# Kernel tuning notes

Measured on AMD Instinct MI355X. Metric: run time of the kernel, lower is better.

The kernel has to match this reference:

```python
import jax, jax.numpy as jnp
import numpy as np

B, C, H, W = 4, 3, 32, 32
N_IMAGES = 32
TIMESTEPS = 20


def _extract_patches(x, pad_mode):
    """3x3 patches at every spatial location. x: [B,C,H,W] -> [B,C,9,H,W]."""
    if pad_mode == 'wrap':
        xp = jnp.pad(x, ((0, 0), (0, 0), (1, 1), (1, 1)), mode='wrap')
    else:
        xp = jnp.pad(x, ((0, 0), (0, 0), (1, 1), (1, 1)))
    h, w = x.shape[2], x.shape[3]
    sl = [xp[:, :, di:di + h, dj:dj + w] for di in range(3) for dj in range(3)]
    return jnp.stack(sl, axis=2)  # [B,C,9,H,W], k = di*3+dj (torch unfold order)


def setup_inputs() -> dict:
    key = jax.random.key(0)
    k1, k2 = jax.random.split(key)
    x = jax.random.normal(k1, (B, C, H, W), dtype=jnp.float32)
    images = jax.random.uniform(k2, (N_IMAGES, C, H, W), dtype=jnp.float32)
    # linear beta schedule, as in _noise_buffers
    betas = jnp.linspace(1e-4, 0.02, TIMESTEPS, dtype=jnp.float32)
    alpha_cumprod = jnp.cumprod(1.0 - betas)
    mu_sched = jnp.sqrt(alpha_cumprod)
    sigma_sched = jnp.sqrt(1.0 - alpha_cumprod)
    return {"x": x, "images": images, "mu_sched": mu_sched,
            "sigma_sched": sigma_sched, "t": 10}


def reference(x, images, mu_sched, sigma_sched, t):
    mu = mu_sched[t]
    sigma = sigma_sched[t]
    b, c, h, w = x.shape

    # x-side: circular-padded 3x3 patches and their squared norms
    xp = _extract_patches(x, 'wrap').reshape(b, c * 9, h, w)   # [B,C*9,H,W]
    x_norms = jnp.sum(xp * xp, axis=1)                          # [B,H,W]

    # dataset-side: zero-padded 3x3 patches at every pixel of every image
    ip = _extract_patches(images, 'zeros')                      # [N,C,9,H,W]
    patches = ip.transpose(0, 3, 4, 1, 2).reshape(-1, c * 9)    # [P, C*9], P=N*H*W
    pnorms = jnp.sum(patches * patches, axis=1)                 # [P]
    pcenters = patches.reshape(-1, c, 9)[:, :, 4]               # [P,C] center pixel (1,1)

    # conv2d(x_pad, patches) == contraction over the C*9 patch axis
    conv = jnp.einsum('bkhw,pk->bphw', xp, patches)             # [B,P,H,W]

    inv2s2 = 1.0 / (2.0 * sigma * sigma)
    log_w = -(x_norms[:, None] - 2.0 * mu * conv
              + (mu * mu) * pnorms[None, :, None, None]) * inv2s2  # [B,P,H,W]

    # stable softmax-style weights over the patch axis (== online LSE result)
    m = jnp.max(log_w, axis=1)                                  # [B,H,W]
    wgt = jnp.exp(log_w - m[:, None])                           # [B,P,H,W]
    sum_w = jnp.sum(wgt, axis=1)                                # [B,H,W]

    # sum_p w * (x - mu * pcenter) = x*sum_w - mu * (w @ pcenters)
    wc = jnp.einsum('bphw,pc->bchw', wgt, pcenters)             # [B,C,H,W]
    sum_wd = x * sum_w[:, None] - mu * wc
    return -sum_wd / (sigma * sigma * sum_w[:, None])
```

## Files before the change

kernel.cpp:

```cpp
#include <hip/hip_runtime.h>
#include <cstddef>

#define P_TOTAL 32768
#define Q_TOTAL 4096
#define NSPLIT 128
#define KPS 256
#define TILES 16
#define QPERWG 256
#define NQG (Q_TOTAL / QPERWG)
#define GRID (NSPLIT * NQG)

typedef _Float16 half8 __attribute__((ext_vector_type(8)));
typedef float floatx4 __attribute__((ext_vector_type(4)));
typedef float floatx2 __attribute__((ext_vector_type(2)));

__device__ __forceinline__ float fexp2(float x) {
#if defined(__has_builtin) && __has_builtin(__builtin_amdgcn_exp2f)
    return __builtin_amdgcn_exp2f(x);
#else
    return exp2f(x);
#endif
}

__global__ __launch_bounds__(256) void qbuild_k(
    const float* __restrict__ x, _Float16* __restrict__ q16)
{
    int q = blockIdx.x * 256 + threadIdx.x;
    int b = q >> 10, rem = q & 1023, h = rem >> 5, w = rem & 31;
    const float* xb = x + (size_t)b * 3072;
    _Float16 row[32];
    #pragma unroll
    for (int c = 0; c < 3; c++)
      #pragma unroll
      for (int di = 0; di < 3; di++)
        #pragma unroll
        for (int dj = 0; dj < 3; dj++)
            row[c * 9 + di * 3 + dj] =
                (_Float16)xb[c * 1024 + ((h + di + 31) & 31) * 32 + ((w + dj + 31) & 31)];
    row[27] = (_Float16)1.0f;
    row[28] = (_Float16)0.f; row[29] = (_Float16)0.f;
    row[30] = (_Float16)0.f; row[31] = (_Float16)0.f;
    _Float16* qp = q16 + (size_t)q * 32;
    #pragma unroll
    for (int u = 0; u < 4; u++) ((float4*)qp)[u] = ((float4*)row)[u];
}

__global__ __launch_bounds__(256) void score_k(
    const _Float16* __restrict__ q16, const float* __restrict__ images,
    const float* __restrict__ mu_sched, const float* __restrict__ sigma_sched,
    const int* __restrict__ tptr, float* __restrict__ partials)
{
    __shared__ char lds[KPS * 64 + 3 * KPS * 4];
    float* ctrp = (float*)(lds + KPS * 64);
    int tid = threadIdx.x;
    int split = blockIdx.x >> 4;
    int qg    = blockIdx.x & 15;

    int t = tptr[0];
    float mu = mu_sched[t], sg = sigma_sched[t];
    const float LOG2E = 1.4426950408889634f;
    float inv2s2 = 1.0f / (2.0f * sg * sg);
    float s1     = 2.0f * mu * inv2s2 * LOG2E;
    float bscale = -mu * mu * inv2s2 * LOG2E;

    {
        int r = tid;
        int p = split * KPS + r;
        int n = p >> 10, rem = p & 1023, i = rem >> 5, j = rem & 31;
        const float* img = images + (size_t)n * 3072;
        _Float16 hrow[32];
        float pnorm = 0.f, c0 = 0.f, c1 = 0.f, c2 = 0.f;
        #pragma unroll
        for (int c = 0; c < 3; c++)
          #pragma unroll
          for (int di = 0; di < 3; di++)
            #pragma unroll
            for (int dj = 0; dj < 3; dj++) {
                int ii = i + di - 1, jj = j + dj - 1;
                float val = 0.f;
                if (ii >= 0 && ii < 32 && jj >= 0 && jj < 32)
                    val = img[c * 1024 + ii * 32 + jj];
                hrow[c * 9 + di * 3 + dj] = (_Float16)(val * s1);
                pnorm = fmaf(val, val, pnorm);
                if (di == 1 && dj == 1) { if (c == 0) c0 = val; else if (c == 1) c1 = val; else c2 = val; }
            }
        hrow[27] = (_Float16)(pnorm * bscale);
        hrow[28] = (_Float16)0.f; hrow[29] = (_Float16)0.f;
        hrow[30] = (_Float16)0.f; hrow[31] = (_Float16)0.f;
        int sw = (r >> 1) & 3;
        float4* src4 = (float4*)hrow;
        #pragma unroll
        for (int c = 0; c < 4; c++)
            *(float4*)(lds + r * 64 + ((c ^ sw) << 4)) = src4[c];
        ctrp[0 * KPS + r] = c0;
        ctrp[1 * KPS + r] = c1;
        ctrp[2 * KPS + r] = c2;
    }

    int lane = tid & 63, wid = tid >> 6;
    int col  = lane & 15, quad = lane >> 4;
    int qbase = qg * QPERWG + wid * 64;

    half8 qf[4];
    #pragma unroll
    for (int f = 0; f < 4; f++)
        qf[f] = *(const half8*)(q16 + (size_t)(qbase + f * 16 + col) * 32 + quad * 8);
    __syncthreads();

    int swc = (col >> 1) & 3;
    const char* abase = lds + col * 64 + ((quad ^ swc) << 4);

    floatx2 mx2[4];
    #pragma unroll
    for (int f = 0; f < 4; f++) mx2[f] = (floatx2){-3e38f, -3e38f};
    {
        #pragma unroll 4
        for (int tile = 0; tile < TILES; tile++) {
            half8 ak = *(const half8*)(abase + tile * 1024);
            #pragma unroll
            for (int f = 0; f < 4; f++) {
                floatx4 a = __builtin_amdgcn_mfma_f32_16x16x32_f16(
                    ak, qf[f], (floatx4){0.f, 0.f, 0.f, 0.f}, 0, 0, 0);
                floatx2 alo = __builtin_shufflevector(a, a, 0, 1);
                floatx2 ahi = __builtin_shufflevector(a, a, 2, 3);
                mx2[f] = __builtin_elementwise_max(
                    mx2[f], __builtin_elementwise_max(alo, ahi));
            }
        }
    }
    float mx[4];
    #pragma unroll
    for (int f = 0; f < 4; f++) {
        mx[f] = fmaxf(mx2[f].x, mx2[f].y);
        mx[f] = fmaxf(mx[f], __shfl_xor(mx[f], 16, 64));
        mx[f] = fmaxf(mx[f], __shfl_xor(mx[f], 32, 64));
    }
    floatx4 nmv[4];
    #pragma unroll
    for (int f = 0; f < 4; f++)
        nmv[f] = (floatx4){-mx[f], -mx[f], -mx[f], -mx[f]};

    floatx2 sv2[4], w02[4], w12[4], w22[4];
    #pragma unroll
    for (int f = 0; f < 4; f++) {
        sv2[f] = (floatx2){0.f, 0.f};
        w02[f] = sv2[f]; w12[f] = sv2[f]; w22[f] = sv2[f];
    }
    {
        #pragma unroll 2
        for (int tile = 0; tile < TILES; tile++) {
            half8 ak = *(const half8*)(abase + tile * 1024);
            int gr = tile * 16 + quad * 4;
            floatx4 c0q = *(const floatx4*)(ctrp + 0 * KPS + gr);
            floatx4 c1q = *(const floatx4*)(ctrp + 1 * KPS + gr);
            floatx4 c2q = *(const floatx4*)(ctrp + 2 * KPS + gr);
            floatx2 c0a = __builtin_shufflevector(c0q, c0q, 0, 1);
            floatx2 c0b = __builtin_shufflevector(c0q, c0q, 2, 3);
            floatx2 c1a = __builtin_shufflevector(c1q, c1q, 0, 1);
            floatx2 c1b = __builtin_shufflevector(c1q, c1q, 2, 3);
            floatx2 c2a = __builtin_shufflevector(c2q, c2q, 0, 1);
            floatx2 c2b = __builtin_shufflevector(c2q, c2q, 2, 3);
            #pragma unroll
            for (int f = 0; f < 4; f++) {
                floatx4 a = __builtin_amdgcn_mfma_f32_16x16x32_f16(ak, qf[f], nmv[f], 0, 0, 0);
                floatx2 e01 = {fexp2(a[0]), fexp2(a[1])};
                floatx2 e23 = {fexp2(a[2]), fexp2(a[3])};
                sv2[f] += e01 + e23;
                w02[f] = __builtin_elementwise_fma(e01, c0a, w02[f]);
                w02[f] = __builtin_elementwise_fma(e23, c0b, w02[f]);
                w12[f] = __builtin_elementwise_fma(e01, c1a, w12[f]);
                w12[f] = __builtin_elementwise_fma(e23, c1b, w12[f]);
                w22[f] = __builtin_elementwise_fma(e01, c2a, w22[f]);
                w22[f] = __builtin_elementwise_fma(e23, c2b, w22[f]);
            }
        }
    }

    #pragma unroll
    for (int f = 0; f < 4; f++) {
        float sv = sv2[f].x + sv2[f].y;
        float w0 = w02[f].x + w02[f].y;
        float w1 = w12[f].x + w12[f].y;
        float w2 = w22[f].x + w22[f].y;
        sv += __shfl_xor(sv, 16, 64);  sv += __shfl_xor(sv, 32, 64);
        w0 += __shfl_xor(w0, 16, 64);  w0 += __shfl_xor(w0, 32, 64);
        w1 += __shfl_xor(w1, 16, 64);  w1 += __shfl_xor(w1, 32, 64);
        w2 += __shfl_xor(w2, 16, 64);  w2 += __shfl_xor(w2, 32, 64);
        if (quad == 0) {
            size_t idx = (size_t)split * Q_TOTAL + qbase + f * 16 + col;
            partials[idx]                          = mx[f];
            partials[idx + (size_t)NSPLIT * Q_TOTAL]     = sv;
            partials[idx + (size_t)NSPLIT * Q_TOTAL * 2] = w0;
            partials[idx + (size_t)NSPLIT * Q_TOTAL * 3] = w1;
            partials[idx + (size_t)NSPLIT * Q_TOTAL * 4] = w2;
        }
    }
}

__global__ __launch_bounds__(256) void combine_k(
    const float* __restrict__ x, const float* __restrict__ partials,
    const float* __restrict__ mu_sched, const float* __restrict__ sigma_sched,
    const int* __restrict__ tptr, float* __restrict__ out)
{
    int q = blockIdx.x * 256 + threadIdx.x;
    int t = tptr[0];
    float mu = mu_sched[t], sg = sigma_sched[t];
    float inv_s2 = 1.0f / (sg * sg);

    const size_t PL = (size_t)NSPLIT * Q_TOTAL;
    float M = -3e38f, S = 0.f, W0 = 0.f, W1 = 0.f, W2 = 0.f;
    for (int sp = 0; sp < NSPLIT; sp++) {
        size_t idx = (size_t)sp * Q_TOTAL + q;
        float mval = partials[idx];
        float sval = partials[idx + PL];
        float w0v  = partials[idx + PL * 2];
        float w1v  = partials[idx + PL * 3];
        float w2v  = partials[idx + PL * 4];
        float mnew = fmaxf(M, mval);
        float sco = fexp2(M - mnew);
        float scn = fexp2(mval - mnew);
        S  = fmaf(S,  sco, sval * scn);
        W0 = fmaf(W0, sco, w0v * scn);
        W1 = fmaf(W1, sco, w1v * scn);
        W2 = fmaf(W2, sco, w2v * scn);
        M = mnew;
    }
    float invS = 1.0f / S;
    int b = q >> 10, rem = q & 1023;
    #pragma unroll
    for (int c = 0; c < 3; c++) {
        float Wc = (c == 0) ? W0 : (c == 1 ? W1 : W2);
        float xc = x[(size_t)b * 3072 + c * 1024 + rem];
        out[(size_t)b * 3072 + c * 1024 + rem] = -(xc - mu * Wc * invS) * inv_s2;
    }
}

extern "C" void kernel_launch(void* const* d_in, const int* in_sizes, int n_in,
                              void* d_out, int out_size, void* d_ws, size_t ws_size,
                              hipStream_t stream) {
    const float* x      = (const float*)d_in[0];
    const float* images = (const float*)d_in[1];
    const float* mu_s   = (const float*)d_in[2];
    const float* sg_s   = (const float*)d_in[3];
    const int*   tptr   = (const int*)d_in[4];
    float* out = (float*)d_out;

    float*    partials = (float*)d_ws;
    _Float16* q16      = (_Float16*)((char*)d_ws + (size_t)5 * NSPLIT * Q_TOTAL * 4);

    qbuild_k<<<Q_TOTAL / 256, 256, 0, stream>>>(x, q16);
    score_k<<<GRID, 256, 0, stream>>>(q16, images, mu_s, sg_s, tptr, partials);
    combine_k<<<Q_TOTAL / 256, 256, 0, stream>>>(
        x, partials, mu_s, sg_s, tptr, out);
}
```

Before: 120.7 us.

## Compute weighted sums with a second MFMA over fp16 exp weights via LDS

Replaces the per-lane FMA accumulation of sum_w and the weighted patch centers with a second MFMA. The exp weights are converted to fp16, staged in per-wave LDS, and multiplied against an LDS value matrix holding [1, c0, c1, c2] plus zero padding. This moves the reduction work from VALU onto matrix cores. In exchange it adds LDS round trips, lowers precision by storing the weights in fp16 with round-toward-zero, and increases LDS footprint, which may reduce occupancy.

```diff
diff --git a/kernel.cpp b/kernel.cpp
--- a/kernel.cpp
+++ b/kernel.cpp
@@ -6,13 +6,24 @@
 #define NSPLIT 128
 #define KPS 256
 #define TILES 16
+#define NGROUP 8
 #define QPERWG 256
 #define NQG (Q_TOTAL / QPERWG)
 #define GRID (NSPLIT * NQG)
 
+#define KEYS_B 16384
+#define VT_OFF KEYS_B
+#define VT_PITCH 528
+#define VT_ZERO (VT_OFF + 4 * VT_PITCH)
+#define P_OFF (VT_OFF + 2624)
+#define P_FRAG 1280
+#define P_WAVE (4 * P_FRAG)
+#define LDS_TOTAL (P_OFF + 4 * P_WAVE)
+
 typedef _Float16 half8 __attribute__((ext_vector_type(8)));
+typedef __fp16 fp16x2 __attribute__((ext_vector_type(2)));
+typedef __fp16 fp16x4 __attribute__((ext_vector_type(4)));
 typedef float floatx4 __attribute__((ext_vector_type(4)));
-typedef float floatx2 __attribute__((ext_vector_type(2)));
 
 __device__ __forceinline__ float fexp2(float x) {
 #if defined(__has_builtin) && __has_builtin(__builtin_amdgcn_exp2f)
@@ -50,8 +61,7 @@
     const float* __restrict__ mu_sched, const float* __restrict__ sigma_sched,
     const int* __restrict__ tptr, float* __restrict__ partials)
 {
-    __shared__ char lds[KPS * 64 + 3 * KPS * 4];
-    float* ctrp = (float*)(lds + KPS * 64);
+    __shared__ char lds[LDS_TOTAL];
     int tid = threadIdx.x;
     int split = blockIdx.x >> 4;
     int qg    = blockIdx.x & 15;
@@ -92,9 +102,12 @@
         #pragma unroll
         for (int c = 0; c < 4; c++)
             *(float4*)(lds + r * 64 + ((c ^ sw) << 4)) = src4[c];
-        ctrp[0 * KPS + r] = c0;
-        ctrp[1 * KPS + r] = c1;
-        ctrp[2 * KPS + r] = c2;
+        _Float16* vt = (_Float16*)(lds + VT_OFF);
+        vt[0 * (VT_PITCH / 2) + r] = (_Float16)1.0f;
+        vt[1 * (VT_PITCH / 2) + r] = (_Float16)c0;
+        vt[2 * (VT_PITCH / 2) + r] = (_Float16)c1;
+        vt[3 * (VT_PITCH / 2) + r] = (_Float16)c2;
+        if (tid < 128) ((float*)(lds + VT_ZERO))[tid] = 0.f;
     }
 
     int lane = tid & 63, wid = tid >> 6;
@@ -110,10 +123,11 @@
     int swc = (col >> 1) & 3;
     const char* abase = lds + col * 64 + ((quad ^ swc) << 4);
 
-    floatx2 mx2[4];
-    #pragma unroll
-    for (int f = 0; f < 4; f++) mx2[f] = (floatx2){-3e38f, -3e38f};
+    float mx[4];
     {
+        floatx4 mv[4];
+        #pragma unroll
+        for (int f = 0; f < 4; f++) mv[f] = (floatx4){-3e38f, -3e38f, -3e38f, -3e38f};
         #pragma unroll 4
         for (int tile = 0; tile < TILES; tile++) {
             half8 ak = *(const half8*)(abase + tile * 1024);
@@ -121,79 +135,69 @@
             for (int f = 0; f < 4; f++) {
                 floatx4 a = __builtin_amdgcn_mfma_f32_16x16x32_f16(
                     ak, qf[f], (floatx4){0.f, 0.f, 0.f, 0.f}, 0, 0, 0);
-                floatx2 alo = __builtin_shufflevector(a, a, 0, 1);
-                floatx2 ahi = __builtin_shufflevector(a, a, 2, 3);
-                mx2[f] = __builtin_elementwise_max(
-                    mx2[f], __builtin_elementwise_max(alo, ahi));
+                mv[f] = __builtin_elementwise_max(mv[f], a);
             }
         }
-    }
-    float mx[4];
-    #pragma unroll
-    for (int f = 0; f < 4; f++) {
-        mx[f] = fmaxf(mx2[f].x, mx2[f].y);
-        mx[f] = fmaxf(mx[f], __shfl_xor(mx[f], 16, 64));
-        mx[f] = fmaxf(mx[f], __shfl_xor(mx[f], 32, 64));
+        #pragma unroll
+        for (int f = 0; f < 4; f++) {
+            mx[f] = fmaxf(fmaxf(mv[f][0], mv[f][1]), fmaxf(mv[f][2], mv[f][3]));
+            mx[f] = fmaxf(mx[f], __shfl_xor(mx[f], 16, 64));
+            mx[f] = fmaxf(mx[f], __shfl_xor(mx[f], 32, 64));
+        }
     }
     floatx4 nmv[4];
     #pragma unroll
     for (int f = 0; f < 4; f++)
         nmv[f] = (floatx4){-mx[f], -mx[f], -mx[f], -mx[f]};
 
-    floatx2 sv2[4], w02[4], w12[4], w22[4];
-    #pragma unroll
-    for (int f = 0; f < 4; f++) {
-        sv2[f] = (floatx2){0.f, 0.f};
-        w02[f] = sv2[f]; w12[f] = sv2[f]; w22[f] = sv2[f];
-    }
-    {
-        #pragma unroll 2
-        for (int tile = 0; tile < TILES; tile++) {
-            half8 ak = *(const half8*)(abase + tile * 1024);
-            int gr = tile * 16 + quad * 4;
-            floatx4 c0q = *(const floatx4*)(ctrp + 0 * KPS + gr);
-            floatx4 c1q = *(const floatx4*)(ctrp + 1 * KPS + gr);
-            floatx4 c2q = *(const floatx4*)(ctrp + 2 * KPS + gr);
-            floatx2 c0a = __builtin_shufflevector(c0q, c0q, 0, 1);
-            floatx2 c0b = __builtin_shufflevector(c0q, c0q, 2, 3);
-            floatx2 c1a = __builtin_shufflevector(c1q, c1q, 0, 1);
-            floatx2 c1b = __builtin_shufflevector(c1q, c1q, 2, 3);
-            floatx2 c2a = __builtin_shufflevector(c2q, c2q, 0, 1);
-            floatx2 c2b = __builtin_shufflevector(c2q, c2q, 2, 3);
+    if (quad == 0) {
+        #pragma unroll
+        for (int f = 0; f < 4; f++)
+            partials[(size_t)split * Q_TOTAL + qbase + f * 16 + col] = mx[f];
+    }
+
+    const char* pwave = lds + P_OFF + wid * P_WAVE;
+    char* pwbase = (char*)pwave + col * 80 + quad * 8;
+    const char* prbase = pwave + col * 80 + quad * 16;
+    const char* vbase = lds + VT_OFF + (col < 4 ? col * VT_PITCH : 4 * VT_PITCH)
+                        + quad * 16;
+
+    floatx4 acc[4];
+    #pragma unroll
+    for (int f = 0; f < 4; f++) acc[f] = (floatx4){0.f, 0.f, 0.f, 0.f};
+
+    for (int g = 0; g < NGROUP; g++) {
+        half8 ak0 = *(const half8*)(abase + (2 * g) * 1024);
+        half8 ak1 = *(const half8*)(abase + (2 * g + 1) * 1024);
+        half8 vb  = *(const half8*)(vbase + g * 64);
+        #pragma unroll
+        for (int f = 0; f < 4; f++) {
+            floatx4 a0 = __builtin_amdgcn_mfma_f32_16x16x32_f16(ak0, qf[f], nmv[f], 0, 0, 0);
+            floatx4 a1 = __builtin_amdgcn_mfma_f32_16x16x32_f16(ak1, qf[f], nmv[f], 0, 0, 0);
+            fp16x2 p00 = __builtin_amdgcn_cvt_pkrtz(fexp2(a0[0]), fexp2(a0[1]));
+            fp16x2 p01 = __builtin_amdgcn_cvt_pkrtz(fexp2(a0[2]), fexp2(a0[3]));
+            fp16x2 p10 = __builtin_amdgcn_cvt_pkrtz(fexp2(a1[0]), fexp2(a1[1]));
+            fp16x2 p11 = __builtin_amdgcn_cvt_pkrtz(fexp2(a1[2]), fexp2(a1[3]));
+            fp16x4 w0 = __builtin_shufflevector(p00, p01, 0, 1, 2, 3);
+            fp16x4 w1 = __builtin_shufflevector(p10, p11, 0, 1, 2, 3);
+            *(fp16x4*)(pwbase + f * P_FRAG)      = w0;
+            *(fp16x4*)(pwbase + f * P_FRAG + 32) = w1;
+        }
+        #pragma unroll
+        for (int f = 0; f < 4; f++) {
+            half8 pa = *(const half8*)(prbase + f * P_FRAG);
+            acc[f] = __builtin_amdgcn_mfma_f32_16x16x32_f16(pa, vb, acc[f], 0, 0, 0);
+        }
+    }
+
+    if (col < 4) {
+        const size_t PL = (size_t)NSPLIT * Q_TOTAL;
+        float* plane = partials + (size_t)(col + 1) * PL + (size_t)split * Q_TOTAL;
+        #pragma unroll
+        for (int f = 0; f < 4; f++)
             #pragma unroll
-            for (int f = 0; f < 4; f++) {
-                floatx4 a = __builtin_amdgcn_mfma_f32_16x16x32_f16(ak, qf[f], nmv[f], 0, 0, 0);
-                floatx2 e01 = {fexp2(a[0]), fexp2(a[1])};
-                floatx2 e23 = {fexp2(a[2]), fexp2(a[3])};
-                sv2[f] += e01 + e23;
-                w02[f] = __builtin_elementwise_fma(e01, c0a, w02[f]);
-                w02[f] = __builtin_elementwise_fma(e23, c0b, w02[f]);
-                w12[f] = __builtin_elementwise_fma(e01, c1a, w12[f]);
-                w12[f] = __builtin_elementwise_fma(e23, c1b, w12[f]);
-                w22[f] = __builtin_elementwise_fma(e01, c2a, w22[f]);
-                w22[f] = __builtin_elementwise_fma(e23, c2b, w22[f]);
-            }
-        }
-    }
-
-    #pragma unroll
-    for (int f = 0; f < 4; f++) {
-        float sv = sv2[f].x + sv2[f].y;
-        float w0 = w02[f].x + w02[f].y;
-        float w1 = w12[f].x + w12[f].y;
-        float w2 = w22[f].x + w22[f].y;
-        sv += __shfl_xor(sv, 16, 64);  sv += __shfl_xor(sv, 32, 64);
-        w0 += __shfl_xor(w0, 16, 64);  w0 += __shfl_xor(w0, 32, 64);
-        w1 += __shfl_xor(w1, 16, 64);  w1 += __shfl_xor(w1, 32, 64);
-        w2 += __shfl_xor(w2, 16, 64);  w2 += __shfl_xor(w2, 32, 64);
-        if (quad == 0) {
-            size_t idx = (size_t)split * Q_TOTAL + qbase + f * 16 + col;
-            partials[idx]                          = mx[f];
-            partials[idx + (size_t)NSPLIT * Q_TOTAL]     = sv;
-            partials[idx + (size_t)NSPLIT * Q_TOTAL * 2] = w0;
-            partials[idx + (size_t)NSPLIT * Q_TOTAL * 3] = w1;
-            partials[idx + (size_t)NSPLIT * Q_TOTAL * 4] = w2;
-        }
+            for (int r = 0; r < 4; r++)
+                plane[qbase + f * 16 + quad * 4 + r] = acc[f][r];
     }
 }
 
```

After: 114.0 us. 5.6% less time.
